# Optimization experiments

Measured on AMD Instinct MI355X. Metric: run time of the kernel, lower is better.

## Reference

```python
import jax, jax.numpy as jnp
import numpy as np

D, M, ALPHA = 64, 512, 7.18
DIM = 1024
B = M * D  # batch: M clusters x D samples each


def setup_inputs() -> dict:
    key = jax.random.key(0)
    outputs = jax.random.normal(key, (B, DIM), dtype=jnp.float32)
    indices = jnp.arange(B, dtype=jnp.int64 if jax.config.jax_enable_x64 else jnp.int32)
    assignment = indices // D  # sample i -> cluster i//D (contiguous blocks of D)
    loss_vector = jnp.zeros((M,), jnp.float32)
    loss_count = jnp.zeros((M,), jnp.float32)
    return {"outputs": outputs, "indices": indices, "assignment": assignment,
            "loss_vector": loss_vector, "loss_count": loss_count}


def reference(outputs, indices, assignment, loss_vector, loss_count):
    outputs = outputs.astype(jnp.float32)
    own = assignment[indices]                              # [B] cluster id per sample
    n = jnp.float32(B)
    # cluster means (each cluster has exactly D samples)
    means = jax.ops.segment_sum(outputs, own, num_segments=M) / D   # [M, DIM]
    # pooled variance: sum ||x_i - mu_{c(i)}||^2 / (N - 1)
    diff_own = outputs - means[own]
    var_sum = jnp.sum(diff_own * diff_own)
    stdev = -2.0 * var_sum / (n - 1.0)                     # the (negative) -2*sigma^2 term
    # squared distances to every cluster mean: [B, M]
    sq = (jnp.sum(outputs * outputs, axis=1)[:, None]
          + jnp.sum(means * means, axis=1)[None, :]
          - 2.0 * outputs @ means.T)
    exps = jnp.exp(sq / stdev)                             # [B, M]
    own_col = own[:, None]
    own_exp = jnp.take_along_axis(exps, own_col, axis=1)[:, 0]
    denom = jnp.sum(exps, axis=1) - own_exp                # sum over mF != own
    sq_own = jnp.take_along_axis(sq, own_col, axis=1)[:, 0]
    log_ratio = sq_own / stdev - ALPHA - jnp.log(denom)    # log(exp(.-alpha)/denom)
    per_loss = jnp.maximum(-log_ratio, 0.0)                # == -clamp(log_ratio, max=0)
    loss = (jnp.sum(per_loss) / n).reshape(1)
    lv = (loss_vector + jax.ops.segment_sum(per_loss, own, num_segments=M)) / n
    lc = loss_count + jax.ops.segment_sum(jnp.ones((B,), jnp.float32), own, num_segments=M)
    variance = var_sum / (n - 1.0)                         # stdev / -2.0 in the original
    return loss, lv, lc, variance
```

## Files before the change

### kernel.cpp

```cpp
#include <hip/hip_runtime.h>
#include <hip/hip_bf16.h>
#include <stdint.h>

#define DIM 1024
#define ALPHA 7.18f
#define INV_N (1.0f/32768.0f)
#define NM1 32767.0f
#define LOG2E 1.44269504088896f
#define LN2 0.693147180559945f

typedef __attribute__((ext_vector_type(8))) short bfrag8;
typedef __attribute__((ext_vector_type(4))) float f32x4;

typedef const __attribute__((address_space(1))) void gv_t;
typedef __attribute__((address_space(3))) void lv_t;

__device__ __forceinline__ unsigned f2bf_bits(float f) {
    unsigned u = __float_as_uint(f);
    return (u + 0x7fffu + ((u >> 16) & 1u)) >> 16;
}

template<int APRIME>
__global__ __launch_bounds__(512)
void k1_colsum(const float* __restrict__ outputs, const int* __restrict__ indices,
               const int* __restrict__ assignment, float* __restrict__ mean_sums,
               unsigned* __restrict__ counts, float* __restrict__ scalars,
               int* __restrict__ own_g, unsigned short* __restrict__ a_bf) {
    __shared__ int sown[64];
    __shared__ int suni;
    __shared__ float4 spart[256];
    __shared__ float ssq[8];
    const int tid = threadIdx.x;
    const int row0 = blockIdx.x * 64;
    if (tid == 0) suni = 1;
    if (tid < 64) {
        int m = assignment[indices[row0 + tid]];
        sown[tid] = m;
        own_g[row0 + tid] = m;
        atomicAdd(&counts[m], 1u);
    }
    __syncthreads();
    if (tid < 63 && sown[tid] != sown[tid + 1]) suni = 0;
    __syncthreads();

    const int c4 = tid & 255;
    const int rh = tid >> 8;
    const float* gp = outputs + (size_t)(row0 + rh * 32) * DIM + c4 * 4;
    const int tt = c4 >> 3, kc = (c4 >> 1) & 3, half = c4 & 1;
    char* abase = (char*)a_bf + (size_t)blockIdx.x * 131072 + tt * 4096 + half * 8;

    float4 s4 = {0.f, 0.f, 0.f, 0.f};
    float sq = 0.f;
    if (suni) {
        #pragma unroll 8
        for (int r = 0; r < 32; ++r) {
            float4 v = *(const float4*)(gp + (size_t)r * DIM);
            sq = fmaf(v.x, v.x, sq); sq = fmaf(v.y, v.y, sq);
            sq = fmaf(v.z, v.z, sq); sq = fmaf(v.w, v.w, sq);
            s4.x += v.x; s4.y += v.y; s4.z += v.z; s4.w += v.w;
            if (APRIME) {
                int rr = rh * 32 + r;
                unsigned lo = f2bf_bits(v.x) | (f2bf_bits(v.y) << 16);
                unsigned hi = f2bf_bits(v.z) | (f2bf_bits(v.w) << 16);
                *(uint2*)(abase + rr * 64 + ((kc ^ ((rr >> 1) & 3)) << 4)) = make_uint2(lo, hi);
            }
        }
        if (rh) spart[c4] = s4;
        __syncthreads();
        if (!rh) {
            float4 o = spart[c4];
            float* dst = mean_sums + (size_t)sown[0] * DIM + c4 * 4;
            atomicAdd(dst + 0, s4.x + o.x);
            atomicAdd(dst + 1, s4.y + o.y);
            atomicAdd(dst + 2, s4.z + o.z);
            atomicAdd(dst + 3, s4.w + o.w);
        }
    } else {
        int curm = sown[rh * 32];
        for (int r = 0; r < 32; ++r) {
            int rr = rh * 32 + r;
            float4 v = *(const float4*)(gp + (size_t)r * DIM);
            int m = sown[rr];
            if (m != curm) {
                float* dst = mean_sums + (size_t)curm * DIM + c4 * 4;
                atomicAdd(dst + 0, s4.x); atomicAdd(dst + 1, s4.y);
                atomicAdd(dst + 2, s4.z); atomicAdd(dst + 3, s4.w);
                s4 = (float4){0.f, 0.f, 0.f, 0.f};
                curm = m;
            }
            sq = fmaf(v.x, v.x, sq); sq = fmaf(v.y, v.y, sq);
            sq = fmaf(v.z, v.z, sq); sq = fmaf(v.w, v.w, sq);
            s4.x += v.x; s4.y += v.y; s4.z += v.z; s4.w += v.w;
            if (APRIME) {
                unsigned lo = f2bf_bits(v.x) | (f2bf_bits(v.y) << 16);
                unsigned hi = f2bf_bits(v.z) | (f2bf_bits(v.w) << 16);
                *(uint2*)(abase + rr * 64 + ((kc ^ ((rr >> 1) & 3)) << 4)) = make_uint2(lo, hi);
            }
        }
        float* dst = mean_sums + (size_t)curm * DIM + c4 * 4;
        atomicAdd(dst + 0, s4.x); atomicAdd(dst + 1, s4.y);
        atomicAdd(dst + 2, s4.z); atomicAdd(dst + 3, s4.w);
    }
    #pragma unroll
    for (int mk = 32; mk; mk >>= 1) sq += __shfl_xor(sq, mk, 64);
    if ((tid & 63) == 0) ssq[tid >> 6] = sq;
    __syncthreads();
    if (tid == 0) {
        float s = 0.f;
        #pragma unroll
        for (int w = 0; w < 8; ++w) s += ssq[w];
        atomicAdd(&scalars[0], s);
    }
}

__global__ __launch_bounds__(256)
void k2_means(const float* __restrict__ mean_sums, const unsigned* __restrict__ counts,
              unsigned short* __restrict__ b_kt, float* __restrict__ msq,
              float* __restrict__ scalars) {
    const int m = blockIdx.x, t = threadIdx.x;
    const float* row = mean_sums + (size_t)m * DIM;
    float4 v = *(const float4*)(row + t * 4);
    float4 mu = {v.x * (1.0f/64.0f), v.y * (1.0f/64.0f), v.z * (1.0f/64.0f), v.w * (1.0f/64.0f)};
    const int tt = t >> 3, kc = (t >> 1) & 3, half = t & 1;
    unsigned lo = f2bf_bits(mu.x) | (f2bf_bits(mu.y) << 16);
    unsigned hi = f2bf_bits(mu.z) | (f2bf_bits(mu.w) << 16);
    *(uint2*)((char*)b_kt + tt * 32768 + m * 64 + ((kc ^ ((m >> 1) & 3)) << 4) + half * 8)
        = make_uint2(lo, hi);
    float sq = fmaf(mu.x, mu.x, fmaf(mu.y, mu.y, fmaf(mu.z, mu.z, mu.w * mu.w)));
    #pragma unroll
    for (int mk = 32; mk; mk >>= 1) sq += __shfl_xor(sq, mk, 64);
    __shared__ float sw[4];
    if ((t & 63) == 0) sw[t >> 6] = sq;
    __syncthreads();
    if (t == 0) {
        float s = sw[0] + sw[1] + sw[2] + sw[3];
        msq[m] = s;
        atomicAdd(&scalars[1], ((float)counts[m] - 128.0f) * s);
    }
}

__global__ __launch_bounds__(512)
void k3_finalize(float* __restrict__ scalars, const float* __restrict__ msq,
                 const unsigned* __restrict__ counts, const float* __restrict__ loss_vector,
                 const float* __restrict__ loss_count, float* __restrict__ msl,
                 float* __restrict__ out) {
    const int t = threadIdx.x;
    float var_sum = scalars[0] + scalars[1];
    float inv_std = -NM1 / (2.0f * var_sum);
    msl[t] = msq[t] * inv_std * LOG2E;
    out[1 + t] = loss_vector[t] * INV_N;
    out[513 + t] = loss_count[t] + (float)counts[t];
    if (t == 0) {
        out[0] = 0.0f;
        out[1025] = var_sum / NM1;
        scalars[2] = inv_std;
    }
}

template<int APRIME>
__global__ __launch_bounds__(512)
void k4_gemm(const float* __restrict__ outputs, const unsigned short* __restrict__ a_bf,
             const unsigned short* __restrict__ b_kt, const float* __restrict__ msl,
             const float* __restrict__ scalars, const int* __restrict__ own_g,
             float* __restrict__ out) {
    __shared__ short lA[2][64 * 32];
    __shared__ short lB[2][512 * 32];
    __shared__ float red_sum[64][4];
    __shared__ float red_own[64][4];

    const int tid  = threadIdx.x;
    const int lane = tid & 63;
    const int wid  = tid >> 6;
    const int wm   = wid >> 2;
    const int wn   = wid & 3;
    const int brow = blockIdx.x * 64;

    const int rA = tid >> 3;
    const int kq = tid & 7;
    const float* gA = outputs + (size_t)(brow + rA) * DIM + kq * 4;
    const int aw_byte = rA * 64 + (((kq >> 1) ^ ((rA >> 1) & 3)) << 4) + ((kq & 1) << 3);

    const int arow = wm * 32 + (lane & 15);
    const int ar_byte = arow * 64 + (((lane >> 4) ^ ((arow >> 1) & 3)) << 4);
    const int bcol = wn * 128 + (lane & 15);
    const int br_byte = bcol * 64 + (((lane >> 4) ^ ((bcol >> 1) & 3)) << 4);

    const char* aprime = (const char*)a_bf + (size_t)blockIdx.x * 131072;
    const char* bbase  = (const char*)b_kt;

    f32x4 acc[2][8];
    #pragma unroll
    for (int i = 0; i < 2; ++i)
        #pragma unroll
        for (int j = 0; j < 8; ++j)
            acc[i][j] = (f32x4){0.f, 0.f, 0.f, 0.f};

    #pragma unroll
    for (int i = 0; i < 4; ++i) {
        const char* gsrc = bbase + (wid * 4 + i) * 1024 + lane * 16;
        char* ldst = (char*)&lB[0][0] + (wid * 4 + i) * 1024;
        __builtin_amdgcn_global_load_lds((gv_t*)gsrc, (lv_t*)ldst, 16, 0, 0);
    }
    if (APRIME) {
        if (wid < 4) {
            const char* gsrc = aprime + wid * 1024 + lane * 16;
            char* ldst = (char*)&lA[0][0] + wid * 1024;
            __builtin_amdgcn_global_load_lds((gv_t*)gsrc, (lv_t*)ldst, 16, 0, 0);
        }
    } else {
        float4 areg = *(const float4*)gA;
        unsigned lo = f2bf_bits(areg.x) | (f2bf_bits(areg.y) << 16);
        unsigned hi = f2bf_bits(areg.z) | (f2bf_bits(areg.w) << 16);
        *(uint2*)((char*)&lA[0][0] + aw_byte) = make_uint2(lo, hi);
    }
    __syncthreads();

    int cur = 0;
    for (int t = 0; t < 32; ++t) {
        const bool has_next = (t + 1) < 32;
        if (has_next) {
            #pragma unroll
            for (int i = 0; i < 4; ++i) {
                const char* gsrc = bbase + (size_t)(t + 1) * 32768 + (wid * 4 + i) * 1024 + lane * 16;
                char* ldst = (char*)&lB[cur ^ 1][0] + (wid * 4 + i) * 1024;
                __builtin_amdgcn_global_load_lds((gv_t*)gsrc, (lv_t*)ldst, 16, 0, 0);
            }
        }
        float4 anext;
        if (APRIME) {
            if (has_next && wid < 4) {
                const char* gsrc = aprime + (size_t)(t + 1) * 4096 + wid * 1024 + lane * 16;
                char* ldst = (char*)&lA[cur ^ 1][0] + wid * 1024;
                __builtin_amdgcn_global_load_lds((gv_t*)gsrc, (lv_t*)ldst, 16, 0, 0);
            }
        } else if (has_next) {
            anext = *(const float4*)(gA + (t + 1) * 32);
        }

        const char* pa = (const char*)&lA[cur][0] + ar_byte;
        const char* pb = (const char*)&lB[cur][0] + br_byte;
        bfrag8 a0 = *(const bfrag8*)(pa);
        bfrag8 a1 = *(const bfrag8*)(pa + 1024);
        #pragma unroll
        for (int fn = 0; fn < 8; ++fn) {
            bfrag8 bf = *(const bfrag8*)(pb + fn * 1024);
            acc[0][fn] = __builtin_amdgcn_mfma_f32_16x16x32_bf16(a0, bf, acc[0][fn], 0, 0, 0);
            acc[1][fn] = __builtin_amdgcn_mfma_f32_16x16x32_bf16(a1, bf, acc[1][fn], 0, 0, 0);
        }

        if (!APRIME && has_next) {
            unsigned lo = f2bf_bits(anext.x) | (f2bf_bits(anext.y) << 16);
            unsigned hi = f2bf_bits(anext.z) | (f2bf_bits(anext.w) << 16);
            *(uint2*)((char*)&lA[cur ^ 1][0] + aw_byte) = make_uint2(lo, hi);
        }
        __syncthreads();
        cur ^= 1;
    }

    float mslv[8];
    #pragma unroll
    for (int fn = 0; fn < 8; ++fn) mslv[fn] = msl[bcol + fn * 16];
    const float inv_std = scalars[2];
    const float c2k = -2.0f * inv_std * LOG2E;
    int ownv[2][4];
    #pragma unroll
    for (int fm = 0; fm < 2; ++fm)
        #pragma unroll
        for (int rg = 0; rg < 4; ++rg)
            ownv[fm][rg] = own_g[brow + wm * 32 + fm * 16 + ((lane >> 4) << 2) + rg];

    #pragma unroll
    for (int fm = 0; fm < 2; ++fm) {
        #pragma unroll
        for (int rg = 0; rg < 4; ++rg) {
            float sum = 0.f, oa = -1e30f;
            int ownr = ownv[fm][rg];
            #pragma unroll
            for (int fn = 0; fn < 8; ++fn) {
                float dot = acc[fm][fn][rg];
                float arg = fmaf(c2k, dot, mslv[fn]);
                sum += exp2f(arg);
                bool isown = (bcol + fn * 16) == ownr;
                oa = isown ? arg : oa;
            }
            #pragma unroll
            for (int mk = 1; mk < 16; mk <<= 1) {
                sum += __shfl_xor(sum, mk, 64);
                oa = fmaxf(oa, __shfl_xor(oa, mk, 64));
            }
            if ((lane & 15) == 0) {
                int r_in = wm * 32 + fm * 16 + ((lane >> 4) << 2) + rg;
                red_sum[r_in][wn] = sum;
                red_own[r_in][wn] = oa;
            }
        }
    }
    __syncthreads();

    if (tid < 64) {
        float s = red_sum[tid][0] + red_sum[tid][1] + red_sum[tid][2] + red_sum[tid][3];
        float oa = fmaxf(fmaxf(red_own[tid][0], red_own[tid][1]),
                         fmaxf(red_own[tid][2], red_own[tid][3]));
        float denom = s - exp2f(oa);
        float per_loss = fmaxf(ALPHA + LN2 * (log2f(denom) - oa), 0.f);
        int ownr = own_g[brow + tid];
        float ls = per_loss;
        #pragma unroll
        for (int mk = 1; mk < 64; mk <<= 1) ls += __shfl_xor(ls, mk, 64);
        int own0 = __shfl(ownr, 0, 64);
        if (__all(ownr == own0)) {
            if (tid == 0) atomicAdd(&out[1 + own0], ls * INV_N);
        } else {
            atomicAdd(&out[1 + ownr], per_loss * INV_N);
        }
        if (tid == 0) atomicAdd(&out[0], ls * INV_N);
    }
}

extern "C" void kernel_launch(void* const* d_in, const int* in_sizes, int n_in,
                              void* d_out, int out_size, void* d_ws, size_t ws_size,
                              hipStream_t stream) {
    const float* outputs     = (const float*)d_in[0];
    const int*   indices     = (const int*)d_in[1];
    const int*   assignment  = (const int*)d_in[2];
    const float* loss_vector = (const float*)d_in[3];
    const float* loss_count  = (const float*)d_in[4];
    float* out = (float*)d_out;

    char* ws = (char*)d_ws;
    float*          mean_sums = (float*)ws;
    unsigned*       counts    = (unsigned*)(ws + 2097152);
    float*          scalars   = (float*)(ws + 2099200);
    const size_t    ZB        = 2099456;
    unsigned short* b_kt      = (unsigned short*)(ws + 2101248);
    float*          msq       = (float*)(ws + 3149824);
    float*          msl       = (float*)(ws + 3151872);
    int*            own_g     = (int*)(ws + 3153920);
    const size_t    A_OFF     = 4194304;
    unsigned short* a_bf      = (unsigned short*)(ws + A_OFF);
    const size_t    NEED      = A_OFF + 67108864ULL;

    hipMemsetAsync(d_ws, 0, ZB, stream);
    if (ws_size >= NEED) {
        hipLaunchKernelGGL((k1_colsum<1>), dim3(512), dim3(512), 0, stream,
                           outputs, indices, assignment, mean_sums, counts, scalars, own_g, a_bf);
        hipLaunchKernelGGL(k2_means, dim3(512), dim3(256), 0, stream,
                           mean_sums, counts, b_kt, msq, scalars);
        hipLaunchKernelGGL(k3_finalize, dim3(1), dim3(512), 0, stream,
                           scalars, msq, counts, loss_vector, loss_count, msl, out);
        hipLaunchKernelGGL((k4_gemm<1>), dim3(512), dim3(512), 0, stream,
                           outputs, a_bf, b_kt, msl, scalars, own_g, out);
    } else {
        hipLaunchKernelGGL((k1_colsum<0>), dim3(512), dim3(512), 0, stream,
                           outputs, indices, assignment, mean_sums, counts, scalars, own_g, a_bf);
        hipLaunchKernelGGL(k2_means, dim3(512), dim3(256), 0, stream,
                           mean_sums, counts, b_kt, msq, scalars);
        hipLaunchKernelGGL(k3_finalize, dim3(1), dim3(512), 0, stream,
                           scalars, msq, counts, loss_vector, loss_count, msl, out);
        hipLaunchKernelGGL((k4_gemm<0>), dim3(512), dim3(512), 0, stream,
                           outputs, a_bf, b_kt, msl, scalars, own_g, out);
    }
}
```

Baseline: 279.5 us.

## Drop bf16 A staging buffer, use 128-row GEMM tiles, split colsum across columns

Removes the precomputed bf16 copy of the activations (64 MB written in k1 and read back in k4). k4 now converts fp32 activations to bf16 inline, with 128-row tiles per block so each B tile loaded into LDS is reused across twice as many rows. k1 splits each 64-row group across 4 blocks by column quarter, giving 2048 smaller blocks for more parallelism. The cost is heavier register and LDS use per GEMM block, fp32 A loads inside the main loop, and only 256 GEMM blocks, which may underfill the device.

```diff
diff --git a/kernel.cpp b/kernel.cpp
--- a/kernel.cpp
+++ b/kernel.cpp
@@ -20,69 +20,61 @@
     return (u + 0x7fffu + ((u >> 16) & 1u)) >> 16;
 }
 
-template<int APRIME>
 __global__ __launch_bounds__(512)
 void k1_colsum(const float* __restrict__ outputs, const int* __restrict__ indices,
                const int* __restrict__ assignment, float* __restrict__ mean_sums,
                unsigned* __restrict__ counts, float* __restrict__ scalars,
-               int* __restrict__ own_g, unsigned short* __restrict__ a_bf) {
+               int* __restrict__ own_g) {
     __shared__ int sown[64];
     __shared__ int suni;
-    __shared__ float4 spart[256];
+    __shared__ float4 spart[8][64];
     __shared__ float ssq[8];
     const int tid = threadIdx.x;
-    const int row0 = blockIdx.x * 64;
+    const int rg = blockIdx.x >> 2, cq = blockIdx.x & 3;
+    const int row0 = rg * 64;
     if (tid == 0) suni = 1;
     if (tid < 64) {
         int m = assignment[indices[row0 + tid]];
         sown[tid] = m;
-        own_g[row0 + tid] = m;
-        atomicAdd(&counts[m], 1u);
+        if (cq == 0) { own_g[row0 + tid] = m; atomicAdd(&counts[m], 1u); }
     }
     __syncthreads();
     if (tid < 63 && sown[tid] != sown[tid + 1]) suni = 0;
     __syncthreads();
 
-    const int c4 = tid & 255;
-    const int rh = tid >> 8;
-    const float* gp = outputs + (size_t)(row0 + rh * 32) * DIM + c4 * 4;
-    const int tt = c4 >> 3, kc = (c4 >> 1) & 3, half = c4 & 1;
-    char* abase = (char*)a_bf + (size_t)blockIdx.x * 131072 + tt * 4096 + half * 8;
-
+    const int c4 = tid & 63;
+    const int rq = tid >> 6;
+    const float* gp = outputs + (size_t)(row0 + rq * 8) * DIM + cq * 256 + c4 * 4;
     float4 s4 = {0.f, 0.f, 0.f, 0.f};
     float sq = 0.f;
+
     if (suni) {
-        #pragma unroll 8
-        for (int r = 0; r < 32; ++r) {
+        #pragma unroll
+        for (int r = 0; r < 8; ++r) {
             float4 v = *(const float4*)(gp + (size_t)r * DIM);
             sq = fmaf(v.x, v.x, sq); sq = fmaf(v.y, v.y, sq);
             sq = fmaf(v.z, v.z, sq); sq = fmaf(v.w, v.w, sq);
             s4.x += v.x; s4.y += v.y; s4.z += v.z; s4.w += v.w;
-            if (APRIME) {
-                int rr = rh * 32 + r;
-                unsigned lo = f2bf_bits(v.x) | (f2bf_bits(v.y) << 16);
-                unsigned hi = f2bf_bits(v.z) | (f2bf_bits(v.w) << 16);
-                *(uint2*)(abase + rr * 64 + ((kc ^ ((rr >> 1) & 3)) << 4)) = make_uint2(lo, hi);
-            }
-        }
-        if (rh) spart[c4] = s4;
+        }
+        spart[rq][c4] = s4;
         __syncthreads();
-        if (!rh) {
-            float4 o = spart[c4];
-            float* dst = mean_sums + (size_t)sown[0] * DIM + c4 * 4;
-            atomicAdd(dst + 0, s4.x + o.x);
-            atomicAdd(dst + 1, s4.y + o.y);
-            atomicAdd(dst + 2, s4.z + o.z);
-            atomicAdd(dst + 3, s4.w + o.w);
+        if (rq == 0) {
+            #pragma unroll
+            for (int r = 1; r < 8; ++r) {
+                float4 o = spart[r][c4];
+                s4.x += o.x; s4.y += o.y; s4.z += o.z; s4.w += o.w;
+            }
+            float* dst = mean_sums + (size_t)sown[0] * DIM + cq * 256 + c4 * 4;
+            atomicAdd(dst + 0, s4.x); atomicAdd(dst + 1, s4.y);
+            atomicAdd(dst + 2, s4.z); atomicAdd(dst + 3, s4.w);
         }
     } else {
-        int curm = sown[rh * 32];
-        for (int r = 0; r < 32; ++r) {
-            int rr = rh * 32 + r;
+        int curm = sown[rq * 8];
+        for (int r = 0; r < 8; ++r) {
             float4 v = *(const float4*)(gp + (size_t)r * DIM);
-            int m = sown[rr];
+            int m = sown[rq * 8 + r];
             if (m != curm) {
-                float* dst = mean_sums + (size_t)curm * DIM + c4 * 4;
+                float* dst = mean_sums + (size_t)curm * DIM + cq * 256 + c4 * 4;
                 atomicAdd(dst + 0, s4.x); atomicAdd(dst + 1, s4.y);
                 atomicAdd(dst + 2, s4.z); atomicAdd(dst + 3, s4.w);
                 s4 = (float4){0.f, 0.f, 0.f, 0.f};
@@ -91,16 +83,13 @@
             sq = fmaf(v.x, v.x, sq); sq = fmaf(v.y, v.y, sq);
             sq = fmaf(v.z, v.z, sq); sq = fmaf(v.w, v.w, sq);
             s4.x += v.x; s4.y += v.y; s4.z += v.z; s4.w += v.w;
-            if (APRIME) {
-                unsigned lo = f2bf_bits(v.x) | (f2bf_bits(v.y) << 16);
-                unsigned hi = f2bf_bits(v.z) | (f2bf_bits(v.w) << 16);
-                *(uint2*)(abase + rr * 64 + ((kc ^ ((rr >> 1) & 3)) << 4)) = make_uint2(lo, hi);
-            }
-        }
-        float* dst = mean_sums + (size_t)curm * DIM + c4 * 4;
+        }
+        float* dst = mean_sums + (size_t)curm * DIM + cq * 256 + c4 * 4;
         atomicAdd(dst + 0, s4.x); atomicAdd(dst + 1, s4.y);
         atomicAdd(dst + 2, s4.z); atomicAdd(dst + 3, s4.w);
-    }
+        __syncthreads();
+    }
+
     #pragma unroll
     for (int mk = 32; mk; mk >>= 1) sq += __shfl_xor(sq, mk, 64);
     if ((tid & 63) == 0) ssq[tid >> 6] = sq;
@@ -157,40 +146,38 @@
     }
 }
 
-template<int APRIME>
-__global__ __launch_bounds__(512)
-void k4_gemm(const float* __restrict__ outputs, const unsigned short* __restrict__ a_bf,
-             const unsigned short* __restrict__ b_kt, const float* __restrict__ msl,
-             const float* __restrict__ scalars, const int* __restrict__ own_g,
-             float* __restrict__ out) {
-    __shared__ short lA[2][64 * 32];
+__global__ __launch_bounds__(512, 2)
+void k4_gemm(const float* __restrict__ outputs, const unsigned short* __restrict__ b_kt,
+             const float* __restrict__ msl, const float* __restrict__ scalars,
+             const int* __restrict__ own_g, float* __restrict__ out) {
+    __shared__ short lA[2][128 * 32];
     __shared__ short lB[2][512 * 32];
-    __shared__ float red_sum[64][4];
-    __shared__ float red_own[64][4];
+    __shared__ float red_sum[128][4];
+    __shared__ float red_own[128][4];
 
     const int tid  = threadIdx.x;
     const int lane = tid & 63;
     const int wid  = tid >> 6;
     const int wm   = wid >> 2;
     const int wn   = wid & 3;
-    const int brow = blockIdx.x * 64;
+    const int brow = blockIdx.x * 128;
 
     const int rA = tid >> 3;
     const int kq = tid & 7;
     const float* gA = outputs + (size_t)(brow + rA) * DIM + kq * 4;
-    const int aw_byte = rA * 64 + (((kq >> 1) ^ ((rA >> 1) & 3)) << 4) + ((kq & 1) << 3);
-
-    const int arow = wm * 32 + (lane & 15);
-    const int ar_byte = arow * 64 + (((lane >> 4) ^ ((arow >> 1) & 3)) << 4);
+    const int aw0 = rA * 64 + ((((kq >> 1)) ^ ((rA >> 1) & 3)) << 4) + ((kq & 1) << 3);
+    const int aw1 = aw0 + 64 * 64;
+
+    const int arow0 = wm * 64 + (lane & 15);
+    const int ar_base = arow0 * 64 + (((lane >> 4) ^ ((arow0 >> 1) & 3)) << 4);
     const int bcol = wn * 128 + (lane & 15);
     const int br_byte = bcol * 64 + (((lane >> 4) ^ ((bcol >> 1) & 3)) << 4);
 
-    const char* aprime = (const char*)a_bf + (size_t)blockIdx.x * 131072;
-    const char* bbase  = (const char*)b_kt;
-
-    f32x4 acc[2][8];
-    #pragma unroll
-    for (int i = 0; i < 2; ++i)
+    const char* bbase = (const char*)b_kt;
+
+    f32x4 acc[4][8];
+    #pragma unroll
+    for (int i = 0; i < 4; ++i)
         #pragma unroll
         for (int j = 0; j < 8; ++j)
             acc[i][j] = (f32x4){0.f, 0.f, 0.f, 0.f};
@@ -201,24 +188,25 @@
         char* ldst = (char*)&lB[0][0] + (wid * 4 + i) * 1024;
         __builtin_amdgcn_global_load_lds((gv_t*)gsrc, (lv_t*)ldst, 16, 0, 0);
     }
-    if (APRIME) {
-        if (wid < 4) {
-            const char* gsrc = aprime + wid * 1024 + lane * 16;
-            char* ldst = (char*)&lA[0][0] + wid * 1024;
-            __builtin_amdgcn_global_load_lds((gv_t*)gsrc, (lv_t*)ldst, 16, 0, 0);
-        }
-    } else {
-        float4 areg = *(const float4*)gA;
-        unsigned lo = f2bf_bits(areg.x) | (f2bf_bits(areg.y) << 16);
-        unsigned hi = f2bf_bits(areg.z) | (f2bf_bits(areg.w) << 16);
-        *(uint2*)((char*)&lA[0][0] + aw_byte) = make_uint2(lo, hi);
+    {
+        float4 a0 = *(const float4*)gA;
+        float4 a1 = *(const float4*)(gA + 64 * DIM);
+        unsigned l0 = f2bf_bits(a0.x) | (f2bf_bits(a0.y) << 16);
+        unsigned h0 = f2bf_bits(a0.z) | (f2bf_bits(a0.w) << 16);
+        unsigned l1 = f2bf_bits(a1.x) | (f2bf_bits(a1.y) << 16);
+        unsigned h1 = f2bf_bits(a1.z) | (f2bf_bits(a1.w) << 16);
+        *(uint2*)((char*)&lA[0][0] + aw0) = make_uint2(l0, h0);
+        *(uint2*)((char*)&lA[0][0] + aw1) = make_uint2(l1, h1);
     }
     __syncthreads();
 
     int cur = 0;
     for (int t = 0; t < 32; ++t) {
         const bool has_next = (t + 1) < 32;
+        float4 a0n, a1n;
         if (has_next) {
+            a0n = *(const float4*)(gA + (t + 1) * 32);
+            a1n = *(const float4*)(gA + 64 * DIM + (t + 1) * 32);
             #pragma unroll
             for (int i = 0; i < 4; ++i) {
                 const char* gsrc = bbase + (size_t)(t + 1) * 32768 + (wid * 4 + i) * 1024 + lane * 16;
@@ -226,32 +214,27 @@
                 __builtin_amdgcn_global_load_lds((gv_t*)gsrc, (lv_t*)ldst, 16, 0, 0);
             }
         }
-        float4 anext;
-        if (APRIME) {
-            if (has_next && wid < 4) {
-                const char* gsrc = aprime + (size_t)(t + 1) * 4096 + wid * 1024 + lane * 16;
-                char* ldst = (char*)&lA[cur ^ 1][0] + wid * 1024;
-                __builtin_amdgcn_global_load_lds((gv_t*)gsrc, (lv_t*)ldst, 16, 0, 0);
-            }
-        } else if (has_next) {
-            anext = *(const float4*)(gA + (t + 1) * 32);
-        }
-
-        const char* pa = (const char*)&lA[cur][0] + ar_byte;
+
+        const char* pa = (const char*)&lA[cur][0] + ar_base;
         const char* pb = (const char*)&lB[cur][0] + br_byte;
-        bfrag8 a0 = *(const bfrag8*)(pa);
-        bfrag8 a1 = *(const bfrag8*)(pa + 1024);
+        bfrag8 af[4];
+        #pragma unroll
+        for (int fm = 0; fm < 4; ++fm) af[fm] = *(const bfrag8*)(pa + fm * 1024);
         #pragma unroll
         for (int fn = 0; fn < 8; ++fn) {
             bfrag8 bf = *(const bfrag8*)(pb + fn * 1024);
-            acc[0][fn] = __builtin_amdgcn_mfma_f32_16x16x32_bf16(a0, bf, acc[0][fn], 0, 0, 0);
-            acc[1][fn] = __builtin_amdgcn_mfma_f32_16x16x32_bf16(a1, bf, acc[1][fn], 0, 0, 0);
-        }
-
-        if (!APRIME && has_next) {
-            unsigned lo = f2bf_bits(anext.x) | (f2bf_bits(anext.y) << 16);
-            unsigned hi = f2bf_bits(anext.z) | (f2bf_bits(anext.w) << 16);
-            *(uint2*)((char*)&lA[cur ^ 1][0] + aw_byte) = make_uint2(lo, hi);
+            #pragma unroll
+            for (int fm = 0; fm < 4; ++fm)
+                acc[fm][fn] = __builtin_amdgcn_mfma_f32_16x16x32_bf16(af[fm], bf, acc[fm][fn], 0, 0, 0);
+        }
+
+        if (has_next) {
+            unsigned l0 = f2bf_bits(a0n.x) | (f2bf_bits(a0n.y) << 16);
+            unsigned h0 = f2bf_bits(a0n.z) | (f2bf_bits(a0n.w) << 16);
+            unsigned l1 = f2bf_bits(a1n.x) | (f2bf_bits(a1n.y) << 16);
+            unsigned h1 = f2bf_bits(a1n.z) | (f2bf_bits(a1n.w) << 16);
+            *(uint2*)((char*)&lA[cur ^ 1][0] + aw0) = make_uint2(l0, h0);
+            *(uint2*)((char*)&lA[cur ^ 1][0] + aw1) = make_uint2(l1, h1);
         }
         __syncthreads();
         cur ^= 1;
@@ -262,15 +245,15 @@
     for (int fn = 0; fn < 8; ++fn) mslv[fn] = msl[bcol + fn * 16];
     const float inv_std = scalars[2];
     const float c2k = -2.0f * inv_std * LOG2E;
-    int ownv[2][4];
-    #pragma unroll
-    for (int fm = 0; fm < 2; ++fm)
+    int ownv[4][4];
+    #pragma unroll
+    for (int fm = 0; fm < 4; ++fm)
         #pragma unroll
         for (int rg = 0; rg < 4; ++rg)
-            ownv[fm][rg] = own_g[brow + wm * 32 + fm * 16 + ((lane >> 4) << 2) + rg];
-
-    #pragma unroll
-    for (int fm = 0; fm < 2; ++fm) {
+            ownv[fm][rg] = own_g[brow + wm * 64 + fm * 16 + ((lane >> 4) << 2) + rg];
+
+    #pragma unroll
+    for (int fm = 0; fm < 4; ++fm) {
         #pragma unroll
         for (int rg = 0; rg < 4; ++rg) {
             float sum = 0.f, oa = -1e30f;
@@ -289,7 +272,7 @@
                 oa = fmaxf(oa, __shfl_xor(oa, mk, 64));
             }
             if ((lane & 15) == 0) {
-                int r_in = wm * 32 + fm * 16 + ((lane >> 4) << 2) + rg;
+                int r_in = wm * 64 + fm * 16 + ((lane >> 4) << 2) + rg;
                 red_sum[r_in][wn] = sum;
                 red_own[r_in][wn] = oa;
             }
@@ -297,7 +280,7 @@
     }
     __syncthreads();
 
-    if (tid < 64) {
+    if (tid < 128) {
         float s = red_sum[tid][0] + red_sum[tid][1] + red_sum[tid][2] + red_sum[tid][3];
         float oa = fmaxf(fmaxf(red_own[tid][0], red_own[tid][1]),
                          fmaxf(red_own[tid][2], red_own[tid][3]));
@@ -309,11 +292,11 @@
         for (int mk = 1; mk < 64; mk <<= 1) ls += __shfl_xor(ls, mk, 64);
         int own0 = __shfl(ownr, 0, 64);
         if (__all(ownr == own0)) {
-            if (tid == 0) atomicAdd(&out[1 + own0], ls * INV_N);
+            if (lane == 0) atomicAdd(&out[1 + own0], ls * INV_N);
         } else {
             atomicAdd(&out[1 + ownr], per_loss * INV_N);
         }
-        if (tid == 0) atomicAdd(&out[0], ls * INV_N);
+        if (lane == 0) atomicAdd(&out[0], ls * INV_N);
     }
 }
 
@@ -336,28 +319,14 @@
     float*          msq       = (float*)(ws + 3149824);
     float*          msl       = (float*)(ws + 3151872);
     int*            own_g     = (int*)(ws + 3153920);
-    const size_t    A_OFF     = 4194304;
-    unsigned short* a_bf      = (unsigned short*)(ws + A_OFF);
-    const size_t    NEED      = A_OFF + 67108864ULL;
 
     hipMemsetAsync(d_ws, 0, ZB, stream);
-    if (ws_size >= NEED) {
-        hipLaunchKernelGGL((k1_colsum<1>), dim3(512), dim3(512), 0, stream,
-                           outputs, indices, assignment, mean_sums, counts, scalars, own_g, a_bf);
-        hipLaunchKernelGGL(k2_means, dim3(512), dim3(256), 0, stream,
-                           mean_sums, counts, b_kt, msq, scalars);
-        hipLaunchKernelGGL(k3_finalize, dim3(1), dim3(512), 0, stream,
-                           scalars, msq, counts, loss_vector, loss_count, msl, out);
-        hipLaunchKernelGGL((k4_gemm<1>), dim3(512), dim3(512), 0, stream,
-                           outputs, a_bf, b_kt, msl, scalars, own_g, out);
-    } else {
-        hipLaunchKernelGGL((k1_colsum<0>), dim3(512), dim3(512), 0, stream,
-                           outputs, indices, assignment, mean_sums, counts, scalars, own_g, a_bf);
-        hipLaunchKernelGGL(k2_means, dim3(512), dim3(256), 0, stream,
-                           mean_sums, counts, b_kt, msq, scalars);
-        hipLaunchKernelGGL(k3_finalize, dim3(1), dim3(512), 0, stream,
-                           scalars, msq, counts, loss_vector, loss_count, msl, out);
-        hipLaunchKernelGGL((k4_gemm<0>), dim3(512), dim3(512), 0, stream,
-                           outputs, a_bf, b_kt, msl, scalars, own_g, out);
-    }
-}
+    hipLaunchKernelGGL(k1_colsum, dim3(2048), dim3(512), 0, stream,
+                       outputs, indices, assignment, mean_sums, counts, scalars, own_g);
+    hipLaunchKernelGGL(k2_means, dim3(512), dim3(256), 0, stream,
+                       mean_sums, counts, b_kt, msq, scalars);
+    hipLaunchKernelGGL(k3_finalize, dim3(1), dim3(512), 0, stream,
+                       scalars, msq, counts, loss_vector, loss_count, msl, out);
+    hipLaunchKernelGGL(k4_gemm, dim3(256), dim3(512), 0, stream,
+                       outputs, b_kt, msl, scalars, own_g, out);
+}
```

Result: slower. 302.8 us (+8.3%).
